# Kernel tuning notes

Measured on AMD Instinct MI355X. Metric: run time of the kernel, lower is better.

The kernel has to match this reference:

```python
import jax, jax.numpy as jnp
import numpy as np


def sobel_kernels_3d(dtype=jnp.float32):
    # Standard 3D Sobel: derivative [-1,0,1] along one axis, smoothing [1,2,1]
    # along the other two. Returns shape (3, 1, 3, 3, 3) in OIDHW layout.
    s = jnp.array([1.0, 2.0, 1.0], dtype=dtype)
    d = jnp.array([-1.0, 0.0, 1.0], dtype=dtype)
    kd = jnp.einsum('i,j,k->ijk', d, s, s)  # d/dD
    kh = jnp.einsum('i,j,k->ijk', s, d, s)  # d/dH
    kw = jnp.einsum('i,j,k->ijk', s, s, d)  # d/dW
    return jnp.stack([kd, kh, kw], axis=0)[:, None]  # (3,1,3,3,3)


def _grad3d(x, kernels):
    # x: (B, C, D, H, W) -> flatten (B*C, 1, D, H, W), conv with padding=1.
    B, C, D, H, W = x.shape
    x_ = x.reshape(B * C, 1, D, H, W)
    return jax.lax.conv_general_dilated(
        x_, kernels.astype(x.dtype),
        window_strides=(1, 1, 1),
        padding=((1, 1), (1, 1), (1, 1)),
        dimension_numbers=('NCDHW', 'OIDHW', 'NCDHW'),
    )  # (B*C, 3, D, H, W)


def setup_inputs() -> dict:
    key = jax.random.key(0)
    k1, k2 = jax.random.split(key)
    shape = (4, 4, 64, 128, 128)
    pred = jax.random.normal(k1, shape, dtype=jnp.float32)
    target = jax.random.normal(k2, shape, dtype=jnp.float32)
    return {"pred": pred, "target": target}


def reference(pred, target):
    kernels = sobel_kernels_3d(pred.dtype)
    grad_pred = _grad3d(pred, kernels)
    grad_target = _grad3d(target, kernels)
    # loss_type == 'l1'
    return jnp.mean(jnp.abs(grad_pred - grad_target))
```

## Files before the change

### kernel.cpp

```cpp
#include <hip/hip_runtime.h>

#define NB 16
#define DD 64
#define HH 128
#define WW 128
#define HW (HH * WW)

constexpr int CD = 2;
constexpr int TH = 8;
constexpr int LZ = CD + 2;
constexpr int LY = TH + 2;
constexpr int PL = LY * WW;
constexpr int NPOS = LZ * LY * (WW / 4);
constexpr int SLOTS = NPOS / 256;
constexpr int NT = 16;
constexpr float INV_COUNT = 1.0f / 50331648.0f;

__global__ void zero_out_kernel(float* out) {
    if (threadIdx.x == 0 && blockIdx.x == 0) out[0] = 0.0f;
}

__global__ __launch_bounds__(256) void sobel_l1_kernel(
    const float* __restrict__ pred,
    const float* __restrict__ target,
    float* __restrict__ out)
{
    __shared__ float t[2][LZ * PL];

    const int tid = threadIdx.x;
    int b = blockIdx.x;
    const int bh   = b & 15; b >>= 4;
    const int half = b & 1;  b >>= 1;
    const int bn   = b;

    const int h0 = bh * TH;
    const int dbase = half * (NT * CD);
    const size_t nbase = (size_t)bn * (size_t)(DD * HW);

    int  soff[SLOTS];
    int  sz[SLOTS];
    bool sokh[SLOTS];
#pragma unroll
    for (int k = 0; k < SLOTS; ++k) {
        const int i  = k * 256 + tid;
        const int q4 = i & 31;
        const int ry = i >> 5;
        const int z  = ry / LY;
        const int y  = ry - z * LY;
        const int gh = h0 - 1 + y;
        sokh[k] = (unsigned)gh < HH;
        soff[k] = min(max(gh, 0), HH - 1) * WW + 4 * q4;
        sz[k]   = z;
    }

    float4 sp[SLOTS], sq[SLOTS];

    auto load_tile = [&](int tau) {
        const int d0 = dbase + tau * CD;
#pragma unroll
        for (int k = 0; k < SLOTS; ++k) {
            const int gd  = d0 - 1 + sz[k];
            const int gdc = min(max(gd, 0), DD - 1);
            const size_t idx = nbase + (size_t)gdc * HW + soff[k];
            sp[k] = *(const float4*)(pred + idx);
            sq[k] = *(const float4*)(target + idx);
        }
    };

    auto store_tile = [&](int tau, float* B) {
        const int d0 = dbase + tau * CD;
#pragma unroll
        for (int k = 0; k < SLOTS; ++k) {
            const int gd = d0 - 1 + sz[k];
            const float m = (sokh[k] && (unsigned)gd < DD) ? 1.0f : 0.0f;
            const int i = k * 256 + tid;
            const float4 v = float4{(sp[k].x - sq[k].x) * m,
                                    (sp[k].y - sq[k].y) * m,
                                    (sp[k].z - sq[k].z) * m,
                                    (sp[k].w - sq[k].w) * m};
            *(float4*)&B[4 * i] = v;
        }
    };

    const int tc = tid & 31;
    const int lh = tid >> 5;

    auto compute_tile = [&](const float* B, float& acc) {
        auto plane_l = [&](int z, float4& A_, float4& Bh_, float4& Bw_) {
            float4 rs[3], rdw[3];
#pragma unroll
            for (int r = 0; r < 3; ++r) {
                const float4 v = *(const float4*)&B[z * PL + (lh + r) * WW + 4 * tc];
                float lm = __shfl_up(v.w, 1, 32);
                float rp = __shfl_down(v.x, 1, 32);
                if (tc == 0)  lm = 0.f;
                if (tc == 31) rp = 0.f;
                rs[r]  = float4{lm  + 2.f * v.x + v.y,
                                v.x + 2.f * v.y + v.z,
                                v.y + 2.f * v.z + v.w,
                                v.z + 2.f * v.w + rp};
                rdw[r] = float4{v.y - lm, v.z - v.x, v.w - v.y, rp - v.z};
            }
            A_  = float4{rs[0].x + 2.f * rs[1].x + rs[2].x,
                         rs[0].y + 2.f * rs[1].y + rs[2].y,
                         rs[0].z + 2.f * rs[1].z + rs[2].z,
                         rs[0].w + 2.f * rs[1].w + rs[2].w};
            Bh_ = float4{rs[2].x - rs[0].x, rs[2].y - rs[0].y,
                         rs[2].z - rs[0].z, rs[2].w - rs[0].w};
            Bw_ = float4{rdw[0].x + 2.f * rdw[1].x + rdw[2].x,
                         rdw[0].y + 2.f * rdw[1].y + rdw[2].y,
                         rdw[0].z + 2.f * rdw[1].z + rdw[2].z,
                         rdw[0].w + 2.f * rdw[1].w + rdw[2].w};
        };

        float4 rA[3], rBh[3], rBw[3];
        plane_l(0, rA[0], rBh[0], rBw[0]);
        plane_l(1, rA[1], rBh[1], rBw[1]);
#pragma unroll
        for (int ld = 0; ld < CD; ++ld) {
            const int s0 = ld % 3, s1 = (ld + 1) % 3, s2 = (ld + 2) % 3;
            plane_l(ld + 2, rA[s2], rBh[s2], rBw[s2]);
            const float4 a0 = rA[s0],  a2 = rA[s2];
            const float4 b0 = rBh[s0], b1 = rBh[s1], b2 = rBh[s2];
            const float4 c0 = rBw[s0], c1 = rBw[s1], c2 = rBw[s2];
            acc += fabsf(a2.x - a0.x) + fabsf(a2.y - a0.y)
                 + fabsf(a2.z - a0.z) + fabsf(a2.w - a0.w);
            acc += fabsf(b0.x + 2.f * b1.x + b2.x) + fabsf(b0.y + 2.f * b1.y + b2.y)
                 + fabsf(b0.z + 2.f * b1.z + b2.z) + fabsf(b0.w + 2.f * b1.w + b2.w);
            acc += fabsf(c0.x + 2.f * c1.x + c2.x) + fabsf(c0.y + 2.f * c1.y + c2.y)
                 + fabsf(c0.z + 2.f * c1.z + c2.z) + fabsf(c0.w + 2.f * c1.w + c2.w);
        }
    };

    float acc = 0.0f;
    load_tile(0);
    store_tile(0, t[0]);
    __syncthreads();
    for (int tau = 0; tau < NT; ++tau) {
        if (tau + 1 < NT) load_tile(tau + 1);
        compute_tile(t[tau & 1], acc);
        if (tau + 1 < NT) store_tile(tau + 1, t[(tau + 1) & 1]);
        __syncthreads();
    }

#pragma unroll
    for (int off = 32; off > 0; off >>= 1)
        acc += __shfl_down(acc, off, 64);
    if ((tid & 63) == 0) t[0][tid >> 6] = acc;
    __syncthreads();
    if (tid == 0) {
        const float s = t[0][0] + t[0][1] + t[0][2] + t[0][3];
        atomicAdd(out, s * INV_COUNT);
    }
}

extern "C" void kernel_launch(void* const* d_in, const int* in_sizes, int n_in,
                              void* d_out, int out_size, void* d_ws, size_t ws_size,
                              hipStream_t stream) {
    const float* pred   = (const float*)d_in[0];
    const float* target = (const float*)d_in[1];
    float* out = (float*)d_out;

    zero_out_kernel<<<1, 64, 0, stream>>>(out);

    const int nblocks = NB * 2 * (HH / TH);
    sobel_l1_kernel<<<nblocks, 256, 0, stream>>>(pred, target, out);
}
```

Measured before the change: 151.9 us.

## Replace LDS-tiled pipeline with direct global loads and register depth rolling

Removes the shared-memory double-buffered tile. Each thread now loads its three neighbouring rows of 8 floats straight from global memory for every depth plane, and rolls the per-plane partial sums through three register slots. The grid becomes 16 rows by 8 depth chunks per volume, which gives more blocks and shorter depth sweeps. The aim is to drop the LDS stores, loads and barriers. In exchange, each input row is read about three times from global memory or cache, and halo planes are reloaded at depth-chunk edges.

```diff
diff --git a/kernel.cpp b/kernel.cpp
--- a/kernel.cpp
+++ b/kernel.cpp
@@ -6,150 +6,152 @@
 #define WW 128
 #define HW (HH * WW)
 
-constexpr int CD = 2;
-constexpr int TH = 8;
-constexpr int LZ = CD + 2;
-constexpr int LY = TH + 2;
-constexpr int PL = LY * WW;
-constexpr int NPOS = LZ * LY * (WW / 4);
-constexpr int SLOTS = NPOS / 256;
-constexpr int NT = 16;
+constexpr int TROWS = 16;
+constexpr int NQ = 8;
+constexpr int QP = DD / NQ;
 constexpr float INV_COUNT = 1.0f / 50331648.0f;
 
 __global__ void zero_out_kernel(float* out) {
     if (threadIdx.x == 0 && blockIdx.x == 0) out[0] = 0.0f;
 }
 
+
+#define ROWPART(D0, D1, LM, RP, RSa, RSb, RWa, RWb)                         \
+    RSa.x = (LM)   + 2.f*D0.x + D0.y;  RSa.y = D0.x + 2.f*D0.y + D0.z;      \
+    RSa.z = D0.y + 2.f*D0.z + D0.w;    RSa.w = D0.z + 2.f*D0.w + D1.x;      \
+    RSb.x = D0.w + 2.f*D1.x + D1.y;    RSb.y = D1.x + 2.f*D1.y + D1.z;      \
+    RSb.z = D1.y + 2.f*D1.z + D1.w;    RSb.w = D1.z + 2.f*D1.w + (RP);      \
+    RWa.x = D0.y - (LM);   RWa.y = D0.z - D0.x;                             \
+    RWa.z = D0.w - D0.y;   RWa.w = D1.x - D0.z;                             \
+    RWb.x = D1.y - D0.w;   RWb.y = D1.z - D1.x;                             \
+    RWb.z = D1.w - D1.y;   RWb.w = (RP) - D1.z;
+
+#define DIFF4(D, A, B, F)                                                   \
+    D.x = (A.x - B.x) * (F); D.y = (A.y - B.y) * (F);                       \
+    D.z = (A.z - B.z) * (F); D.w = (A.w - B.w) * (F);
+
+#define PARTIALS(...) PARTIALS_IMPL(__VA_ARGS__)
+#define PARTIALS_IMPL(REL, MD, Aa, Ab, Ha, Hb, Wa, Wb) do {                 \
+    const int pc_ = min(max(d0 + (REL), 0), DD - 1);                        \
+    const float* pp_ = pred   + nbase + (size_t)pc_ * HW;                   \
+    const float* pt_ = target + nbase + (size_t)pc_ * HW;                   \
+    const float4 am0_ = *(const float4*)(pp_ + ro_m);                       \
+    const float4 am1_ = *(const float4*)(pp_ + ro_m + 4);                   \
+    const float4 a00_ = *(const float4*)(pp_ + ro_0);                       \
+    const float4 a01_ = *(const float4*)(pp_ + ro_0 + 4);                   \
+    const float4 ap0_ = *(const float4*)(pp_ + ro_p);                       \
+    const float4 ap1_ = *(const float4*)(pp_ + ro_p + 4);                   \
+    const float4 bm0_ = *(const float4*)(pt_ + ro_m);                       \
+    const float4 bm1_ = *(const float4*)(pt_ + ro_m + 4);                   \
+    const float4 b00_ = *(const float4*)(pt_ + ro_0);                       \
+    const float4 b01_ = *(const float4*)(pt_ + ro_0 + 4);                   \
+    const float4 bp0_ = *(const float4*)(pt_ + ro_p);                       \
+    const float4 bp1_ = *(const float4*)(pt_ + ro_p + 4);                   \
+    const float fm_ = mr_m * (MD), f0_ = (MD), fp_ = mr_p * (MD);           \
+    float4 dm0_, dm1_, d00_, d01_, dp0_, dp1_;                              \
+    DIFF4(dm0_, am0_, bm0_, fm_) DIFF4(dm1_, am1_, bm1_, fm_)               \
+    DIFF4(d00_, a00_, b00_, f0_) DIFF4(d01_, a01_, b01_, f0_)               \
+    DIFF4(dp0_, ap0_, bp0_, fp_) DIFF4(dp1_, ap1_, bp1_, fp_)               \
+    const float lmm_ = __shfl_up(dm1_.w, 1, 16) * lmask;                    \
+    const float rpm_ = __shfl_down(dm0_.x, 1, 16) * rmask;                  \
+    const float lm0_ = __shfl_up(d01_.w, 1, 16) * lmask;                    \
+    const float rp0_ = __shfl_down(d00_.x, 1, 16) * rmask;                  \
+    const float lmp_ = __shfl_up(dp1_.w, 1, 16) * lmask;                    \
+    const float rpp_ = __shfl_down(dp0_.x, 1, 16) * rmask;                  \
+    float4 sma_, smb_, wma_, wmb_;                                          \
+    float4 s0a_, s0b_, w0a_, w0b_;                                          \
+    float4 spa_, spb_, wpa_, wpb_;                                          \
+    ROWPART(dm0_, dm1_, lmm_, rpm_, sma_, smb_, wma_, wmb_)                 \
+    ROWPART(d00_, d01_, lm0_, rp0_, s0a_, s0b_, w0a_, w0b_)                 \
+    ROWPART(dp0_, dp1_, lmp_, rpp_, spa_, spb_, wpa_, wpb_)                 \
+    Aa.x = sma_.x + 2.f*s0a_.x + spa_.x;  Aa.y = sma_.y + 2.f*s0a_.y + spa_.y; \
+    Aa.z = sma_.z + 2.f*s0a_.z + spa_.z;  Aa.w = sma_.w + 2.f*s0a_.w + spa_.w; \
+    Ab.x = smb_.x + 2.f*s0b_.x + spb_.x;  Ab.y = smb_.y + 2.f*s0b_.y + spb_.y; \
+    Ab.z = smb_.z + 2.f*s0b_.z + spb_.z;  Ab.w = smb_.w + 2.f*s0b_.w + spb_.w; \
+    Ha.x = spa_.x - sma_.x;  Ha.y = spa_.y - sma_.y;                        \
+    Ha.z = spa_.z - sma_.z;  Ha.w = spa_.w - sma_.w;                        \
+    Hb.x = spb_.x - smb_.x;  Hb.y = spb_.y - smb_.y;                        \
+    Hb.z = spb_.z - smb_.z;  Hb.w = spb_.w - smb_.w;                        \
+    Wa.x = wma_.x + 2.f*w0a_.x + wpa_.x;  Wa.y = wma_.y + 2.f*w0a_.y + wpa_.y; \
+    Wa.z = wma_.z + 2.f*w0a_.z + wpa_.z;  Wa.w = wma_.w + 2.f*w0a_.w + wpa_.w; \
+    Wb.x = wmb_.x + 2.f*w0b_.x + wpb_.x;  Wb.y = wmb_.y + 2.f*w0b_.y + wpb_.y; \
+    Wb.z = wmb_.z + 2.f*w0b_.z + wpb_.z;  Wb.w = wmb_.w + 2.f*w0b_.w + wpb_.w; \
+} while (0)
+
+#define EMIT(...) EMIT_IMPL(__VA_ARGS__)
+#define EMIT_IMPL(A0a,A0b,H0a,H0b,W0a,W0b, A1a,A1b,H1a,H1b,W1a,W1b, A2a,A2b,H2a,H2b,W2a,W2b) do { \
+    acc += fabsf(A2a.x - A0a.x) + fabsf(A2a.y - A0a.y)                      \
+         + fabsf(A2a.z - A0a.z) + fabsf(A2a.w - A0a.w);                     \
+    acc += fabsf(A2b.x - A0b.x) + fabsf(A2b.y - A0b.y)                      \
+         + fabsf(A2b.z - A0b.z) + fabsf(A2b.w - A0b.w);                     \
+    acc += fabsf(H0a.x + 2.f*H1a.x + H2a.x) + fabsf(H0a.y + 2.f*H1a.y + H2a.y) \
+         + fabsf(H0a.z + 2.f*H1a.z + H2a.z) + fabsf(H0a.w + 2.f*H1a.w + H2a.w); \
+    acc += fabsf(H0b.x + 2.f*H1b.x + H2b.x) + fabsf(H0b.y + 2.f*H1b.y + H2b.y) \
+         + fabsf(H0b.z + 2.f*H1b.z + H2b.z) + fabsf(H0b.w + 2.f*H1b.w + H2b.w); \
+    acc += fabsf(W0a.x + 2.f*W1a.x + W2a.x) + fabsf(W0a.y + 2.f*W1a.y + W2a.y) \
+         + fabsf(W0a.z + 2.f*W1a.z + W2a.z) + fabsf(W0a.w + 2.f*W1a.w + W2a.w); \
+    acc += fabsf(W0b.x + 2.f*W1b.x + W2b.x) + fabsf(W0b.y + 2.f*W1b.y + W2b.y) \
+         + fabsf(W0b.z + 2.f*W1b.z + W2b.z) + fabsf(W0b.w + 2.f*W1b.w + W2b.w); \
+} while (0)
+
+#define SLOT0 c0Aa,c0Ab,c0Ha,c0Hb,c0Wa,c0Wb
+#define SLOT1 c1Aa,c1Ab,c1Ha,c1Hb,c1Wa,c1Wb
+#define SLOT2 c2Aa,c2Ab,c2Ha,c2Hb,c2Wa,c2Wb
+
 __global__ __launch_bounds__(256) void sobel_l1_kernel(
     const float* __restrict__ pred,
     const float* __restrict__ target,
     float* __restrict__ out)
 {
-    __shared__ float t[2][LZ * PL];
+    __shared__ float wsum[4];
 
     const int tid = threadIdx.x;
     int b = blockIdx.x;
-    const int bh   = b & 15; b >>= 4;
-    const int half = b & 1;  b >>= 1;
-    const int bn   = b;
+    const int bh = b & 7;  b >>= 3;
+    const int q  = b & 7;  b >>= 3;
+    const int bn = b;
 
-    const int h0 = bh * TH;
-    const int dbase = half * (NT * CD);
+    const int row = tid >> 4;
+    const int sc  = tid & 15;
+    const int gh  = bh * TROWS + row;
+    const int d0  = q * QP;
     const size_t nbase = (size_t)bn * (size_t)(DD * HW);
 
-    int  soff[SLOTS];
-    int  sz[SLOTS];
-    bool sokh[SLOTS];
-#pragma unroll
-    for (int k = 0; k < SLOTS; ++k) {
-        const int i  = k * 256 + tid;
-        const int q4 = i & 31;
-        const int ry = i >> 5;
-        const int z  = ry / LY;
-        const int y  = ry - z * LY;
-        const int gh = h0 - 1 + y;
-        sokh[k] = (unsigned)gh < HH;
-        soff[k] = min(max(gh, 0), HH - 1) * WW + 4 * q4;
-        sz[k]   = z;
-    }
+    const int wq   = sc * 8;
+    const int ro_m = max(gh - 1, 0) * WW + wq;
+    const int ro_0 = gh * WW + wq;
+    const int ro_p = min(gh + 1, HH - 1) * WW + wq;
+    const float mr_m = (gh - 1 >= 0) ? 1.f : 0.f;
+    const float mr_p = (gh + 1 < HH) ? 1.f : 0.f;
+    const float lmask = (sc == 0)  ? 0.f : 1.f;
+    const float rmask = (sc == 15) ? 0.f : 1.f;
+    const float mdA = (q == 0)      ? 0.f : 1.f;
+    const float mdB = (q == NQ - 1) ? 0.f : 1.f;
 
-    float4 sp[SLOTS], sq[SLOTS];
+    float acc = 0.f;
 
-    auto load_tile = [&](int tau) {
-        const int d0 = dbase + tau * CD;
-#pragma unroll
-        for (int k = 0; k < SLOTS; ++k) {
-            const int gd  = d0 - 1 + sz[k];
-            const int gdc = min(max(gd, 0), DD - 1);
-            const size_t idx = nbase + (size_t)gdc * HW + soff[k];
-            sp[k] = *(const float4*)(pred + idx);
-            sq[k] = *(const float4*)(target + idx);
-        }
-    };
+    float4 c0Aa, c0Ab, c0Ha, c0Hb, c0Wa, c0Wb;
+    float4 c1Aa, c1Ab, c1Ha, c1Hb, c1Wa, c1Wb;
+    float4 c2Aa, c2Ab, c2Ha, c2Hb, c2Wa, c2Wb;
 
-    auto store_tile = [&](int tau, float* B) {
-        const int d0 = dbase + tau * CD;
-#pragma unroll
-        for (int k = 0; k < SLOTS; ++k) {
-            const int gd = d0 - 1 + sz[k];
-            const float m = (sokh[k] && (unsigned)gd < DD) ? 1.0f : 0.0f;
-            const int i = k * 256 + tid;
-            const float4 v = float4{(sp[k].x - sq[k].x) * m,
-                                    (sp[k].y - sq[k].y) * m,
-                                    (sp[k].z - sq[k].z) * m,
-                                    (sp[k].w - sq[k].w) * m};
-            *(float4*)&B[4 * i] = v;
-        }
-    };
-
-    const int tc = tid & 31;
-    const int lh = tid >> 5;
-
-    auto compute_tile = [&](const float* B, float& acc) {
-        auto plane_l = [&](int z, float4& A_, float4& Bh_, float4& Bw_) {
-            float4 rs[3], rdw[3];
-#pragma unroll
-            for (int r = 0; r < 3; ++r) {
-                const float4 v = *(const float4*)&B[z * PL + (lh + r) * WW + 4 * tc];
-                float lm = __shfl_up(v.w, 1, 32);
-                float rp = __shfl_down(v.x, 1, 32);
-                if (tc == 0)  lm = 0.f;
-                if (tc == 31) rp = 0.f;
-                rs[r]  = float4{lm  + 2.f * v.x + v.y,
-                                v.x + 2.f * v.y + v.z,
-                                v.y + 2.f * v.z + v.w,
-                                v.z + 2.f * v.w + rp};
-                rdw[r] = float4{v.y - lm, v.z - v.x, v.w - v.y, rp - v.z};
-            }
-            A_  = float4{rs[0].x + 2.f * rs[1].x + rs[2].x,
-                         rs[0].y + 2.f * rs[1].y + rs[2].y,
-                         rs[0].z + 2.f * rs[1].z + rs[2].z,
-                         rs[0].w + 2.f * rs[1].w + rs[2].w};
-            Bh_ = float4{rs[2].x - rs[0].x, rs[2].y - rs[0].y,
-                         rs[2].z - rs[0].z, rs[2].w - rs[0].w};
-            Bw_ = float4{rdw[0].x + 2.f * rdw[1].x + rdw[2].x,
-                         rdw[0].y + 2.f * rdw[1].y + rdw[2].y,
-                         rdw[0].z + 2.f * rdw[1].z + rdw[2].z,
-                         rdw[0].w + 2.f * rdw[1].w + rdw[2].w};
-        };
-
-        float4 rA[3], rBh[3], rBw[3];
-        plane_l(0, rA[0], rBh[0], rBw[0]);
-        plane_l(1, rA[1], rBh[1], rBw[1]);
-#pragma unroll
-        for (int ld = 0; ld < CD; ++ld) {
-            const int s0 = ld % 3, s1 = (ld + 1) % 3, s2 = (ld + 2) % 3;
-            plane_l(ld + 2, rA[s2], rBh[s2], rBw[s2]);
-            const float4 a0 = rA[s0],  a2 = rA[s2];
-            const float4 b0 = rBh[s0], b1 = rBh[s1], b2 = rBh[s2];
-            const float4 c0 = rBw[s0], c1 = rBw[s1], c2 = rBw[s2];
-            acc += fabsf(a2.x - a0.x) + fabsf(a2.y - a0.y)
-                 + fabsf(a2.z - a0.z) + fabsf(a2.w - a0.w);
-            acc += fabsf(b0.x + 2.f * b1.x + b2.x) + fabsf(b0.y + 2.f * b1.y + b2.y)
-                 + fabsf(b0.z + 2.f * b1.z + b2.z) + fabsf(b0.w + 2.f * b1.w + b2.w);
-            acc += fabsf(c0.x + 2.f * c1.x + c2.x) + fabsf(c0.y + 2.f * c1.y + c2.y)
-                 + fabsf(c0.z + 2.f * c1.z + c2.z) + fabsf(c0.w + 2.f * c1.w + c2.w);
-        }
-    };
-
-    float acc = 0.0f;
-    load_tile(0);
-    store_tile(0, t[0]);
-    __syncthreads();
-    for (int tau = 0; tau < NT; ++tau) {
-        if (tau + 1 < NT) load_tile(tau + 1);
-        compute_tile(t[tau & 1], acc);
-        if (tau + 1 < NT) store_tile(tau + 1, t[(tau + 1) & 1]);
-        __syncthreads();
-    }
+    PARTIALS(-1, mdA, SLOT0);
+    PARTIALS( 0, 1.f, SLOT1);
+    PARTIALS( 1, 1.f, SLOT2);  EMIT(SLOT0, SLOT1, SLOT2);
+    PARTIALS( 2, 1.f, SLOT0);  EMIT(SLOT1, SLOT2, SLOT0);
+    PARTIALS( 3, 1.f, SLOT1);  EMIT(SLOT2, SLOT0, SLOT1);
+    PARTIALS( 4, 1.f, SLOT2);  EMIT(SLOT0, SLOT1, SLOT2);
+    PARTIALS( 5, 1.f, SLOT0);  EMIT(SLOT1, SLOT2, SLOT0);
+    PARTIALS( 6, 1.f, SLOT1);  EMIT(SLOT2, SLOT0, SLOT1);
+    PARTIALS( 7, 1.f, SLOT2);  EMIT(SLOT0, SLOT1, SLOT2);
+    PARTIALS( 8, mdB, SLOT0);  EMIT(SLOT1, SLOT2, SLOT0);
 
 #pragma unroll
     for (int off = 32; off > 0; off >>= 1)
         acc += __shfl_down(acc, off, 64);
-    if ((tid & 63) == 0) t[0][tid >> 6] = acc;
+    if ((tid & 63) == 0) wsum[tid >> 6] = acc;
     __syncthreads();
     if (tid == 0) {
-        const float s = t[0][0] + t[0][1] + t[0][2] + t[0][3];
+        const float s = wsum[0] + wsum[1] + wsum[2] + wsum[3];
         atomicAdd(out, s * INV_COUNT);
     }
 }
@@ -163,6 +165,6 @@
 
     zero_out_kernel<<<1, 64, 0, stream>>>(out);
 
-    const int nblocks = NB * 2 * (HH / TH);
+    const int nblocks = NB * NQ * (HH / TROWS);
     sobel_l1_kernel<<<nblocks, 256, 0, stream>>>(pred, target, out);
 }
```

Measured after the change: 156.7 us. +3.2%, slower.
